# Performance work log

Measured on AMD Instinct MI355X. Metric: run time of the kernel, lower is better.

## Reference

```python
import jax, jax.numpy as jnp
import numpy as np

MAX_SEP_LEN = 512  # tables have 2*MAX_SEP_LEN+1 = 1025 rows


def setup_inputs() -> dict:
    key = jax.random.key(0)
    ks = jax.random.split(key, 8)
    B, S, H = 4, 256, 160
    T = 2 * MAX_SEP_LEN + 1
    return {
        "pos_s": jax.random.randint(ks[0], (B, S), 0, MAX_SEP_LEN),
        "pos_e": jax.random.randint(ks[1], (B, S), 0, MAX_SEP_LEN),
        "pe_ss": jax.random.normal(ks[2], (T, H), dtype=jnp.float32),
        "pe_se": jax.random.normal(ks[3], (T, H), dtype=jnp.float32),
        "pe_es": jax.random.normal(ks[4], (T, H), dtype=jnp.float32),
        "pe_ee": jax.random.normal(ks[5], (T, H), dtype=jnp.float32),
        "W": jax.random.normal(ks[6], (H, 4 * H), dtype=jnp.float32) * 0.02,
        "b": jax.random.normal(ks[7], (H,), dtype=jnp.float32) * 0.02,
    }


def reference(pos_s, pos_e, pe_ss, pe_se, pe_es, pe_ee, W, b):
    # relative position indices, offset into table range [0, 2*MAX_SEP_LEN]
    d_ss = pos_s[:, :, None] - pos_s[:, None, :] + MAX_SEP_LEN  # [B,S,S]
    d_se = pos_s[:, :, None] - pos_e[:, None, :] + MAX_SEP_LEN
    d_es = pos_e[:, :, None] - pos_s[:, None, :] + MAX_SEP_LEN
    d_ee = pos_e[:, :, None] - pos_e[:, None, :] + MAX_SEP_LEN
    # gathers: [B,S,S,H] each
    x = jnp.concatenate(
        [pe_ss[d_ss], pe_se[d_se], pe_es[d_es], pe_ee[d_ee]], axis=-1
    )  # [B,S,S,4H]
    # fused Linear(4H -> H) + ReLU
    out = jnp.einsum("bijk,hk->bijh", x, W) + b
    return jax.nn.relu(out)
```

## Files before the change

### kernel.cpp

```cpp
#include <hip/hip_runtime.h>

#define MAX_SEP 512
#define T_ROWS 1025
#define H 160
#define B 4
#define S 256
#define HV (H/4)

__global__ __launch_bounds__(256) void transpose_w(const float* __restrict__ W,
                                                   float* __restrict__ Wt) {
    int g = blockIdx.x * 256 + threadIdx.x;
    if (g >= 4 * H * H) return;
    int h  = g % H;
    int kk = (g / H) % H;
    int q  = g / (H * H);
    Wt[g] = W[h * (4 * H) + q * H + kk];
}

#define TG 257

__global__ __launch_bounds__(256) void compute_y(
        const float* __restrict__ pe0, const float* __restrict__ pe1,
        const float* __restrict__ pe2, const float* __restrict__ pe3,
        const float* __restrict__ Wt,  const float* __restrict__ bias,
        float* __restrict__ Y) {
    int e = blockIdx.x * 256 + threadIdx.x;
    if (e >= 4 * TG * H) return;
    int h  = e % H;
    int tg = (e / H) % TG;
    int q  = e / (H * TG);
    const float* pe = (q == 0) ? pe0 : (q == 1) ? pe1 : (q == 2) ? pe2 : pe3;

    int t0 = tg * 4;
    int t1 = min(t0 + 1, T_ROWS - 1);
    int t2 = min(t0 + 2, T_ROWS - 1);
    int t3 = min(t0 + 3, T_ROWS - 1);
    const float* p0 = pe + (size_t)t0 * H;
    const float* p1 = pe + (size_t)t1 * H;
    const float* p2 = pe + (size_t)t2 * H;
    const float* p3 = pe + (size_t)t3 * H;
    const float* wt = Wt + (size_t)q * H * H + h;

    float a0 = 0.f, a1 = 0.f, a2 = 0.f, a3 = 0.f;
#pragma unroll 8
    for (int kk = 0; kk < H; ++kk) {
        float w = wt[(size_t)kk * H];
        a0 = fmaf(p0[kk], w, a0);
        a1 = fmaf(p1[kk], w, a1);
        a2 = fmaf(p2[kk], w, a2);
        a3 = fmaf(p3[kk], w, a3);
    }
    float bb = (q == 0) ? bias[h] : 0.f;
    float* yq = Y + ((size_t)q * T_ROWS + t0) * H + h;
    yq[0] = a0 + bb;
    if (t0 + 1 < T_ROWS) yq[H]     = a1 + bb;
    if (t0 + 2 < T_ROWS) yq[2 * H] = a2 + bb;
    if (t0 + 3 < T_ROWS) yq[3 * H] = a3 + bb;
}

__global__ __launch_bounds__(256) void gather_add(
        const int* __restrict__ pos_s, const int* __restrict__ pos_e,
        const float* __restrict__ Y, float* __restrict__ out) {
    int bi = blockIdx.x;
    int bb = bi / S;
    int i  = bi % S;
    int tid = threadIdx.x;

    __shared__ int ls[S], le[S];
    ls[tid] = pos_s[bb * S + tid];
    le[tid] = pos_e[bb * S + tid];
    __syncthreads();

    int psi = ls[i];
    int pei = le[i];

    const float4* __restrict__ Y4 = (const float4*)Y;
    float4* __restrict__ out4 = (float4*)out + (size_t)bi * S * HV;

#pragma unroll 4
    for (int base = tid; base < S * HV; base += 256) {
        int j  = base / HV;
        int hv = base - j * HV;
        int pj_s = ls[j], pj_e = le[j];
        int d0 = psi - pj_s + MAX_SEP;
        int d1 = psi - pj_e + MAX_SEP;
        int d2 = pei - pj_s + MAX_SEP;
        int d3 = pei - pj_e + MAX_SEP;
        float4 v0 = Y4[(size_t)(0 * T_ROWS + d0) * HV + hv];
        float4 v1 = Y4[(size_t)(1 * T_ROWS + d1) * HV + hv];
        float4 v2 = Y4[(size_t)(2 * T_ROWS + d2) * HV + hv];
        float4 v3 = Y4[(size_t)(3 * T_ROWS + d3) * HV + hv];
        float4 r;
        r.x = fmaxf(v0.x + v1.x + v2.x + v3.x, 0.f);
        r.y = fmaxf(v0.y + v1.y + v2.y + v3.y, 0.f);
        r.z = fmaxf(v0.z + v1.z + v2.z + v3.z, 0.f);
        r.w = fmaxf(v0.w + v1.w + v2.w + v3.w, 0.f);
        out4[base] = r;
    }
}

extern "C" void kernel_launch(void* const* d_in, const int* in_sizes, int n_in,
                              void* d_out, int out_size, void* d_ws, size_t ws_size,
                              hipStream_t stream) {
    const int*   pos_s = (const int*)d_in[0];
    const int*   pos_e = (const int*)d_in[1];
    const float* pe_ss = (const float*)d_in[2];
    const float* pe_se = (const float*)d_in[3];
    const float* pe_es = (const float*)d_in[4];
    const float* pe_ee = (const float*)d_in[5];
    const float* W     = (const float*)d_in[6];
    const float* bias  = (const float*)d_in[7];
    float* out = (float*)d_out;

    float* Wt = (float*)d_ws;
    float* Y  = Wt + 4 * H * H;

    transpose_w<<<(4 * H * H + 255) / 256, 256, 0, stream>>>(W, Wt);
    compute_y<<<(4 * TG * H + 255) / 256, 256, 0, stream>>>(
        pe_ss, pe_se, pe_es, pe_ee, Wt, bias, Y);
    gather_add<<<B * S, 256, 0, stream>>>(pos_s, pos_e, Y, out);
}
```

Baseline: 211.0 us.

## Drop W transpose, split gather blocks fourfold, use nontemporal output stores

```diff
diff --git a/kernel.cpp b/kernel.cpp
--- a/kernel.cpp
+++ b/kernel.cpp
@@ -5,24 +5,15 @@
 #define H 160
 #define B 4
 #define S 256
-#define HV (H/4)
+#define HV 40
+#define TG 257
 
-__global__ __launch_bounds__(256) void transpose_w(const float* __restrict__ W,
-                                                   float* __restrict__ Wt) {
-    int g = blockIdx.x * 256 + threadIdx.x;
-    if (g >= 4 * H * H) return;
-    int h  = g % H;
-    int kk = (g / H) % H;
-    int q  = g / (H * H);
-    Wt[g] = W[h * (4 * H) + q * H + kk];
-}
-
-#define TG 257
+typedef float v4f __attribute__((ext_vector_type(4)));
 
 __global__ __launch_bounds__(256) void compute_y(
         const float* __restrict__ pe0, const float* __restrict__ pe1,
         const float* __restrict__ pe2, const float* __restrict__ pe3,
-        const float* __restrict__ Wt,  const float* __restrict__ bias,
+        const float* __restrict__ W,   const float* __restrict__ bias,
         float* __restrict__ Y) {
     int e = blockIdx.x * 256 + threadIdx.x;
     if (e >= 4 * TG * H) return;
@@ -39,12 +30,12 @@
     const float* p1 = pe + (size_t)t1 * H;
     const float* p2 = pe + (size_t)t2 * H;
     const float* p3 = pe + (size_t)t3 * H;
-    const float* wt = Wt + (size_t)q * H * H + h;
+    const float* wrow = W + (size_t)h * (4 * H) + q * H;
 
     float a0 = 0.f, a1 = 0.f, a2 = 0.f, a3 = 0.f;
 #pragma unroll 8
     for (int kk = 0; kk < H; ++kk) {
-        float w = wt[(size_t)kk * H];
+        float w = wrow[kk];
         a0 = fmaf(p0[kk], w, a0);
         a1 = fmaf(p1[kk], w, a1);
         a2 = fmaf(p2[kk], w, a2);
@@ -61,9 +52,11 @@
 __global__ __launch_bounds__(256) void gather_add(
         const int* __restrict__ pos_s, const int* __restrict__ pos_e,
         const float* __restrict__ Y, float* __restrict__ out) {
-    int bi = blockIdx.x;
-    int bb = bi / S;
-    int i  = bi % S;
+    int blk = blockIdx.x;
+    int bi  = blk >> 2;
+    int q4  = blk & 3;
+    int bb  = bi >> 8;
+    int i   = bi & (S - 1);
     int tid = threadIdx.x;
 
     __shared__ int ls[S], le[S];
@@ -74,11 +67,12 @@
     int psi = ls[i];
     int pei = le[i];
 
-    const float4* __restrict__ Y4 = (const float4*)Y;
-    float4* __restrict__ out4 = (float4*)out + (size_t)bi * S * HV;
+    const v4f* __restrict__ Y4 = (const v4f*)Y;
+    v4f* __restrict__ out4 = (v4f*)out + (size_t)bi * (S * HV);
 
-#pragma unroll 4
-    for (int base = tid; base < S * HV; base += 256) {
+#pragma unroll 2
+    for (int it = 0; it < 10; ++it) {
+        int base = q4 * 2560 + it * 256 + tid;
         int j  = base / HV;
         int hv = base - j * HV;
         int pj_s = ls[j], pj_e = le[j];
@@ -86,16 +80,17 @@
         int d1 = psi - pj_e + MAX_SEP;
         int d2 = pei - pj_s + MAX_SEP;
         int d3 = pei - pj_e + MAX_SEP;
-        float4 v0 = Y4[(size_t)(0 * T_ROWS + d0) * HV + hv];
-        float4 v1 = Y4[(size_t)(1 * T_ROWS + d1) * HV + hv];
-        float4 v2 = Y4[(size_t)(2 * T_ROWS + d2) * HV + hv];
-        float4 v3 = Y4[(size_t)(3 * T_ROWS + d3) * HV + hv];
-        float4 r;
-        r.x = fmaxf(v0.x + v1.x + v2.x + v3.x, 0.f);
-        r.y = fmaxf(v0.y + v1.y + v2.y + v3.y, 0.f);
-        r.z = fmaxf(v0.z + v1.z + v2.z + v3.z, 0.f);
-        r.w = fmaxf(v0.w + v1.w + v2.w + v3.w, 0.f);
-        out4[base] = r;
+        v4f v0 = Y4[(size_t)(0 * T_ROWS + d0) * HV + hv];
+        v4f v1 = Y4[(size_t)(1 * T_ROWS + d1) * HV + hv];
+        v4f v2 = Y4[(size_t)(2 * T_ROWS + d2) * HV + hv];
+        v4f v3 = Y4[(size_t)(3 * T_ROWS + d3) * HV + hv];
+        v4f s = v0 + v1 + v2 + v3;
+        v4f r;
+        r.x = fmaxf(s.x, 0.f);
+        r.y = fmaxf(s.y, 0.f);
+        r.z = fmaxf(s.z, 0.f);
+        r.w = fmaxf(s.w, 0.f);
+        __builtin_nontemporal_store(r, &out4[base]);
     }
 }
 
@@ -112,11 +107,9 @@
     const float* bias  = (const float*)d_in[7];
     float* out = (float*)d_out;
 
-    float* Wt = (float*)d_ws;
-    float* Y  = Wt + 4 * H * H;
+    float* Y = (float*)d_ws;
 
-    transpose_w<<<(4 * H * H + 255) / 256, 256, 0, stream>>>(W, Wt);
     compute_y<<<(4 * TG * H + 255) / 256, 256, 0, stream>>>(
-        pe_ss, pe_se, pe_es, pe_ee, Wt, bias, Y);
-    gather_add<<<B * S, 256, 0, stream>>>(pos_s, pos_e, Y, out);
+        pe_ss, pe_se, pe_es, pe_ee, W, bias, Y);
+    gather_add<<<4 * B * S, 256, 0, stream>>>(pos_s, pos_e, Y, out);
 }
```

Result: slower. 224.4 us (+6.4%).
